# Performance work log

Hardware: AMD Instinct MI355X
Metric: run time of the kernel (lower is better)

Reference implementation:

```python
import math
import jax, jax.numpy as jnp
import numpy as np

NUM_HEADS = 32
NUM_KV_HEADS = 8
HEAD_SIZE = 128
FEATURE_DIM = 64
SEQ_LEN = 2048
WINDOW_SIZE = 64
EPS = 1e-12
MASK_VALUE = -100000000.0


def _make_masks(n: int, w: int):
    # block-diagonal ones(w,w) tiles, plus the rolled (sub-diagonal) tiles
    m = math.ceil(n / w)
    mask = np.kron(np.eye(m), np.ones((w, w)))
    mask = mask + np.roll(mask, -w, axis=-1)
    mask = mask[:n, :n]
    mask_window = np.tril(mask).astype(bool)[None, None]          # [1,1,n,n]
    mask_linear = np.tril(1.0 - mask).astype(bool)[None, None]    # [1,1,n,n]
    return jnp.asarray(mask_window), jnp.asarray(mask_linear)


def _feature_map(w, x):
    # f(x) = clamp(cat(softmax(xW), softmax(-xW)), min=eps)
    z = jnp.einsum('hdf,bhld->bhlf', w, x)
    return jnp.clip(
        jnp.concatenate([jax.nn.softmax(z, axis=-1), jax.nn.softmax(-z, axis=-1)], axis=-1),
        EPS, None)


def setup_inputs() -> dict:
    key = jax.random.key(0)
    ks = jax.random.split(key, 6)
    return {
        'query': jax.random.normal(ks[0], (SEQ_LEN, NUM_HEADS * HEAD_SIZE), dtype=jnp.float32),
        'key': jax.random.normal(ks[1], (SEQ_LEN, NUM_KV_HEADS * HEAD_SIZE), dtype=jnp.float32),
        'value': jax.random.normal(ks[2], (SEQ_LEN, NUM_KV_HEADS * HEAD_SIZE), dtype=jnp.float32),
        'fmap_q_w': 0.02 * jax.random.normal(ks[3], (NUM_HEADS, HEAD_SIZE, FEATURE_DIM), dtype=jnp.float32),
        'fmap_k_w': 0.02 * jax.random.normal(ks[4], (NUM_HEADS, HEAD_SIZE, FEATURE_DIM), dtype=jnp.float32),
        'window_factors': jax.random.normal(ks[5], (1, NUM_HEADS, 1, 1), dtype=jnp.float32),
    }


def reference(query, key, value, fmap_q_w, fmap_k_w, window_factors):
    T = query.shape[0]
    q = query.reshape(T, NUM_HEADS, HEAD_SIZE)
    k = key.reshape(T, NUM_KV_HEADS, HEAD_SIZE)
    v = value.reshape(T, NUM_KV_HEADS, HEAD_SIZE)
    rep = NUM_HEADS // NUM_KV_HEADS
    k = jnp.repeat(k, rep, axis=1)
    v = jnp.repeat(v, rep, axis=1)
    # [T,H,D] -> [1,H,T,D]
    q = jnp.moveaxis(q, 0, -2)[None]
    k = jnp.moveaxis(k, 0, -2)[None]
    v = jnp.moveaxis(v, 0, -2)[None]

    f_q = _feature_map(fmap_q_w, q)  # [1,H,T,2F]
    f_k = _feature_map(fmap_k_w, k)
    wf = jax.nn.sigmoid(window_factors)

    mask_window, mask_linear = _make_masks(SEQ_LEN, WINDOW_SIZE)
    mask_window = mask_window[:, :, :T, :T]
    mask_linear = mask_linear[:, :, :T, :T]

    # sliding-window softmax term
    a_sm = jnp.einsum('bhmd,bhnd->bhmn', q, k) * (HEAD_SIZE ** -0.5)
    a_sm = jnp.where(mask_window, a_sm, MASK_VALUE)
    a_sm_max = jnp.max(a_sm, axis=-1, keepdims=True)
    a_sm = wf * jnp.exp(a_sm - a_sm_max)
    sum_sm = jnp.sum(a_sm, axis=-1, keepdims=True)

    # linear feature-map term (linear_factor = 1)
    a_ln = jnp.einsum('bhmd,bhnd->bhmn', f_q, f_k)
    a_ln = jnp.where(mask_linear, a_ln, 0.0)
    sum_ln = jnp.sum(a_ln, axis=-1, keepdims=True)

    y = jnp.einsum('bhmn,bhnd->bhmd', a_sm + a_ln, v)
    return y / (sum_sm + sum_ln)
```

## Files before the change

### kernel.cpp

```cpp
#include <hip/hip_runtime.h>
#include <math.h>

#define T_SEQ 2048
#define NH    32
#define NKV   8
#define HS    128
#define FD    64
#define NBLK  32
#define SCAN_NB 30
#define EPSF  1e-12f
#define LDP   136
#define STP   129

typedef unsigned short u16;
typedef __bf16 bf16x8 __attribute__((ext_vector_type(8)));
typedef float  f32x4  __attribute__((ext_vector_type(4)));

__device__ __forceinline__ u16 f2b(float f) {
  unsigned u = __builtin_bit_cast(unsigned, f);
  return (u16)((u + 0x7fffu + ((u >> 16) & 1u)) >> 16);
}

#define FKT_OFF 0
#define ST_OFF  16777216
#define VT_OFF  54525952
#define WT_OFF  58720256
#define KB_OFF  59768832

__device__ __forceinline__ void stage_bf(u16* buf, const u16* __restrict__ src, int tid) {
#pragma unroll
  for (int i = 0; i < 4; ++i) {
    int idx = tid * 8 + i * 2048, rr = idx >> 7, c = idx & 127;
    *(uint4*)(buf + rr * LDP + c) = *(const uint4*)(src + idx);
  }
}
__device__ __forceinline__ void stage_vt(u16* buf, const u16* __restrict__ vts,
                                         int rofs, int kb0, int B, int tid) {
#pragma unroll
  for (int i = 0; i < 4; ++i) {
    int idx = tid * 8 + i * 2048, rr = idx >> 7, c = idx & 127;
    int key = (c < 64) ? (kb0 * 64 + c) : (B * 64 + (c - 64));
    *(uint4*)(buf + rr * LDP + c) = *(const uint4*)(vts + (size_t)(rr + rofs) * T_SEQ + key);
  }
}

__global__ __launch_bounds__(256) void k_prep(
    const float* __restrict__ wq, const float* __restrict__ wk,
    const float* __restrict__ vg, const float* __restrict__ kg,
    u16* __restrict__ WT, u16* __restrict__ VT,
    u16* __restrict__ FKT, u16* __restrict__ KBB)
{
  __shared__ __align__(16) u16 smem[2 * 64 * 136];
  const int bx = blockIdx.x, tid = threadIdx.x;
  const int lane = tid & 63, w = tid >> 6;
  const int quad = lane >> 4, txn = lane & 15;

  if (bx < 32) {
    float* sB = (float*)smem;
    const float* src = wq + (size_t)bx * HS * FD;
    for (int idx = tid * 4; idx < 8192; idx += 1024) {
      int r = idx >> 6, c = idx & 63;
      *(float4*)(sB + r * 68 + c) = *(const float4*)(src + idx);
    }
    __syncthreads();
    u16* dst = WT + (size_t)bx * 8192;
    for (int i = 0; i < 8; ++i) {
      int ch = tid + i * 256;
      int f = ch >> 5, d4 = (ch & 31) * 4;
      ushort4 u;
      u.x = f2b(sB[(d4 + 0) * 68 + f]);
      u.y = f2b(sB[(d4 + 1) * 68 + f]);
      u.z = f2b(sB[(d4 + 2) * 68 + f]);
      u.w = f2b(sB[(d4 + 3) * 68 + f]);
      *(ushort4*)(dst + f * 128 + d4) = u;
    }
    return;
  }

  if (bx < 288) {
    const int idx2 = bx - 32;
    const int b = idx2 & 31, kvh = idx2 >> 5;
    float* sV = (float*)smem;
    for (int idx = tid * 4; idx < 8192; idx += 1024) {
      int r = idx >> 7, c = idx & 127;
      *(float4*)(sV + r * 129 + c) = *(const float4*)(vg + (size_t)(b * 64 + r) * (NKV * HS) + kvh * HS + c);
    }
    __syncthreads();
#pragma unroll
    for (int i = 0; i < 32; ++i) {
      int d = w * 32 + i;
      VT[((size_t)(kvh * 128 + d)) * T_SEQ + b * 64 + lane] = f2b(sV[lane * 129 + d]);
    }
    return;
  }

  const int j2 = bx - 288;
  const int lt = j2 & 31, h = j2 >> 5;
  u16* sX = smem;
  u16* sW = smem + 64 * 136;

  const float* xbase = kg + (h >> 2) * HS;
  const int    xstr  = NKV * HS;
  for (int idx = tid * 4; idx < 8192; idx += 1024) {
    int r = idx >> 7, c = idx & 127;
    float4 v4 = *(const float4*)(xbase + (size_t)(lt * 64 + r) * xstr + c);
    ushort4 u; u.x = f2b(v4.x); u.y = f2b(v4.y); u.z = f2b(v4.z); u.w = f2b(v4.w);
    *(ushort4*)(sX + r * 136 + c) = u;
  }
  {
    const float* wsrc = wk + (size_t)h * (HS * FD);
    const int d = tid >> 1, f0 = (tid & 1) * 32;
#pragma unroll
    for (int i = 0; i < 8; ++i) {
      float4 v4 = *(const float4*)(wsrc + d * 64 + f0 + i * 4);
      sW[(f0 + i * 4 + 0) * 136 + d] = f2b(v4.x);
      sW[(f0 + i * 4 + 1) * 136 + d] = f2b(v4.y);
      sW[(f0 + i * 4 + 2) * 136 + d] = f2b(v4.z);
      sW[(f0 + i * 4 + 3) * 136 + d] = f2b(v4.w);
    }
  }
  __syncthreads();

  if ((h & 3) == 0) {
    u16* ob = KBB + ((size_t)((h >> 2) * NBLK + lt)) * 8192;
    for (int i = 0; i < 4; ++i) {
      int ch = tid + i * 256;
      int row = ch >> 4, d8 = (ch & 15) * 8;
      *(uint4*)(ob + row * 128 + d8) = *(const uint4*)(sX + row * 136 + d8);
    }
  }

  const int arow = w * 16 + txn;
  const f32x4 vzero = {0.f, 0.f, 0.f, 0.f};
  f32x4 zt[4] = {vzero, vzero, vzero, vzero};
#pragma unroll
  for (int ks = 0; ks < 4; ++ks) {
    bf16x8 a = *(const bf16x8*)(sX + arow * 136 + ks * 32 + quad * 8);
#pragma unroll
    for (int nt = 0; nt < 4; ++nt) {
      bf16x8 bb = *(const bf16x8*)(sW + (nt * 16 + txn) * 136 + ks * 32 + quad * 8);
      zt[nt] = __builtin_amdgcn_mfma_f32_16x16x32_bf16(a, bb, zt[nt], 0, 0, 0);
    }
  }

  float E1[4][4], E2[4][4];
#pragma unroll
  for (int r = 0; r < 4; ++r) {
    float zv[4];
    float mx = -1e30f, mn = 1e30f;
#pragma unroll
    for (int nt = 0; nt < 4; ++nt) {
      zv[nt] = zt[nt][r];
      mx = fmaxf(mx, zv[nt]); mn = fminf(mn, zv[nt]);
    }
#pragma unroll
    for (int o = 1; o < 16; o <<= 1) {
      mx = fmaxf(mx, __shfl_xor(mx, o));
      mn = fminf(mn, __shfl_xor(mn, o));
    }
    float e1[4], e2[4], s1 = 0.f, s2 = 0.f;
#pragma unroll
    for (int nt = 0; nt < 4; ++nt) {
      e1[nt] = __expf(zv[nt] - mx); s1 += e1[nt];
      e2[nt] = __expf(mn - zv[nt]); s2 += e2[nt];
    }
#pragma unroll
    for (int o = 1; o < 16; o <<= 1) { s1 += __shfl_xor(s1, o); s2 += __shfl_xor(s2, o); }
    float r1 = 1.f / s1, r2 = 1.f / s2;
#pragma unroll
    for (int nt = 0; nt < 4; ++nt) {
      E1[r][nt] = fmaxf(e1[nt] * r1, EPSF);
      E2[r][nt] = fmaxf(e2[nt] * r2, EPSF);
    }
  }

  __syncthreads();

#pragma unroll
  for (int r = 0; r < 4; ++r) {
    int j = w * 16 + quad * 4 + r;
#pragma unroll
    for (int nt = 0; nt < 4; ++nt) {
      sX[(nt * 16 + txn) * 68 + j]        = f2b(E1[r][nt]);
      sX[(nt * 16 + txn + 64) * 68 + j]   = f2b(E2[r][nt]);
    }
  }
  __syncthreads();
  u16* ob = FKT + ((size_t)(h * 32 + lt)) * 8192;
  for (int i = 0; i < 8; ++i) {
    int ch = tid + i * 256;
    int row = ch >> 4, j4 = (ch & 15) * 4;
    *(ushort4*)(ob + row * 64 + j4) = *(const ushort4*)(sX + row * 68 + j4);
  }
}

__global__ __launch_bounds__(256) void k_scan(
    const u16* __restrict__ FKT, const u16* __restrict__ VT, u16* __restrict__ ST)
{
  __shared__ __align__(16) u16 sVT[2][16 * 72];
  __shared__ __align__(16) u16 sFK[2][64 * 72];
  const int L = blockIdx.x + 8 * blockIdx.y + 16 * blockIdx.z;
  const int xcd = L & 7, j = L >> 3;
  const int hsub = j & 3, fh = (j >> 2) & 1, dc = j >> 3;
  const int h = xcd * 4 + hsub;
  const int tid = threadIdx.x, lane = tid & 63, w = tid >> 6;
  const int quad = lane >> 4, txn = lane & 15;
  const bool doz = (dc == 0);

  bf16x8 vone;
#pragma unroll
  for (int jj = 0; jj < 8; ++jj) vone[jj] = (__bf16)1.0f;

  const u16* vbase = VT + ((size_t)((h >> 2) * 128 + dc * 16)) * T_SEQ;
  const u16* fbase = FKT + (size_t)(h * 32) * 8192 + fh * 4096;

  const int srow = tid >> 4, sj4 = (tid & 15) * 4;
  ushort4 rv, rf[4];
  rv = *(const ushort4*)(vbase + (size_t)srow * T_SEQ + sj4);
#pragma unroll
  for (int i = 0; i < 4; ++i) {
    int ch = tid + i * 256;
    int fr = ch >> 4, fj4 = (ch & 15) * 4;
    rf[i] = *(const ushort4*)(fbase + fr * 64 + fj4);
  }

  const f32x4 vzero = {0.f, 0.f, 0.f, 0.f};
  f32x4 acc = vzero, zacc = vzero;
  int cur = 0;

  for (int b = 0; b < SCAN_NB; ++b) {
    u16* dV = sVT[cur];
    u16* dF = sFK[cur];
    *(ushort4*)(dV + srow * 72 + sj4) = rv;
#pragma unroll
    for (int i = 0; i < 4; ++i) {
      int ch = tid + i * 256;
      int fr = ch >> 4, fj4 = (ch & 15) * 4;
      *(ushort4*)(dF + fr * 72 + fj4) = rf[i];
    }
    __syncthreads();
    if (b + 1 < SCAN_NB) {
      rv = *(const ushort4*)(vbase + (size_t)srow * T_SEQ + (b + 1) * 64 + sj4);
#pragma unroll
      for (int i = 0; i < 4; ++i) {
        int ch = tid + i * 256;
        int fr = ch >> 4, fj4 = (ch & 15) * 4;
        rf[i] = *(const ushort4*)(fbase + (size_t)(b + 1) * 8192 + fr * 64 + fj4);
      }
    }
#pragma unroll
    for (int ks = 0; ks < 2; ++ks) {
      bf16x8 a  = *(const bf16x8*)(dV + txn * 72 + ks * 32 + quad * 8);
      bf16x8 bb = *(const bf16x8*)(dF + (w * 16 + txn) * 72 + ks * 32 + quad * 8);
      acc = __builtin_amdgcn_mfma_f32_16x16x32_bf16(a, bb, acc, 0, 0, 0);
      if (doz) zacc = __builtin_amdgcn_mfma_f32_16x16x32_bf16(vone, bb, zacc, 0, 0, 0);
    }
    u16* Sb = ST + (((size_t)(h * NBLK + b)) * STP + dc * 16) * 128 + fh * 64;
#pragma unroll
    for (int r = 0; r < 4; ++r)
      Sb[(quad * 4 + r) * 128 + w * 16 + txn] = f2b(acc[r]);
    if (doz && quad == 0)
      ST[(((size_t)(h * NBLK + b)) * STP + 128) * 128 + fh * 64 + w * 16 + txn] = f2b(zacc[0]);
    cur ^= 1;
  }
}

__global__ __launch_bounds__(256, 4) void k_main(
    const float* __restrict__ qg, const u16* __restrict__ KBB,
    const u16* __restrict__ WT, const u16* __restrict__ ST,
    const u16* __restrict__ VT, const float* __restrict__ wfac,
    float* __restrict__ out)
{
  __shared__ __align__(16) u16 RA[64 * LDP];
  __shared__ __align__(16) u16 RB[64 * LDP];
  __shared__ __align__(16) u16 sz[128];
  const int L = blockIdx.x + 32 * blockIdx.y;
  const int xcd = L & 7, jj = L >> 3;
  const int hsub = jj & 3, B = jj >> 2;
  const int h = xcd * 4 + hsub;
  const int tid = threadIdx.x;
  const int lane = tid & 63, w = tid >> 6;
  const int quad = lane >> 4, txn = lane & 15;
  const int arow = w * 16 + txn;
  const int koff = quad * 8;

  const f32x4 vzero = {0.f, 0.f, 0.f, 0.f};
  f32x4 y[8];
#pragma unroll
  for (int t = 0; t < 8; ++t) y[t] = vzero;
  float sln[4] = {0.f, 0.f, 0.f, 0.f};
  const bf16x8 bzero = {0, 0, 0, 0, 0, 0, 0, 0};

  const int kb0 = (B >= 1) ? B - 1 : 0;
  const u16* ktB = KBB + ((size_t)((h >> 2) * NBLK + B)) * 8192;
  const u16* ktP = KBB + ((size_t)((h >> 2) * NBLK + kb0)) * 8192;
  const u16* vts = VT  + (size_t)((h >> 2) * 128) * T_SEQ;
  const u16* wqt = WT  + (size_t)h * 8192;
  const u16* ssrc = ST + ((size_t)(h * NBLK + (B >= 2 ? B - 2 : 0))) * (STP * 128);

  {
    const float* qb = qg + (size_t)(B * 64 + w * 16) * (NH * HS) + h * HS;
#pragma unroll
    for (int i = 0; i < 8; ++i) {
      int idx = lane + i * 64;
      int r = idx >> 5, c4 = (idx & 31) * 4;
      float4 v4 = *(const float4*)(qb + (size_t)r * (NH * HS) + c4);
      ushort4 u; u.x = f2b(v4.x); u.y = f2b(v4.y); u.z = f2b(v4.z); u.w = f2b(v4.w);
      *(ushort4*)(RA + (w * 16 + r) * LDP + c4) = u;
    }
  }
  stage_bf(RB, ktB, tid);

  f32x4 zt[4] = {vzero, vzero, vzero, vzero};
  if (B >= 2) {
#pragma unroll
    for (int ks = 0; ks < 4; ++ks) {
      bf16x8 a = *(const bf16x8*)(RA + arow * LDP + ks * 32 + koff);
#pragma unroll
      for (int nt = 0; nt < 4; ++nt) {
        bf16x8 bb = *(const bf16x8*)(wqt + (nt * 16 + txn) * 128 + ks * 32 + koff);
        zt[nt] = __builtin_amdgcn_mfma_f32_16x16x32_bf16(a, bb, zt[nt], 0, 0, 0);
      }
    }
  }

  unsigned Epk[4][4];
  if (B >= 2) {
#pragma unroll
    for (int r = 0; r < 4; ++r) {
      float zv[4];
      float mx = -1e30f, mn = 1e30f;
#pragma unroll
      for (int nt = 0; nt < 4; ++nt) {
        zv[nt] = zt[nt][r];
        mx = fmaxf(mx, zv[nt]); mn = fminf(mn, zv[nt]);
      }
#pragma unroll
      for (int o = 1; o < 16; o <<= 1) {
        mx = fmaxf(mx, __shfl_xor(mx, o));
        mn = fminf(mn, __shfl_xor(mn, o));
      }
      float e1[4], e2[4], s1 = 0.f, s2 = 0.f;
#pragma unroll
      for (int nt = 0; nt < 4; ++nt) {
        e1[nt] = __expf(zv[nt] - mx); s1 += e1[nt];
        e2[nt] = __expf(mn - zv[nt]); s2 += e2[nt];
      }
#pragma unroll
      for (int o = 1; o < 16; o <<= 1) { s1 += __shfl_xor(s1, o); s2 += __shfl_xor(s2, o); }
      float r1 = 1.f / s1, r2 = 1.f / s2;
#pragma unroll
      for (int nt = 0; nt < 4; ++nt) {
        unsigned lo = f2b(fmaxf(e1[nt] * r1, EPSF));
        unsigned hi = f2b(fmaxf(e2[nt] * r2, EPSF));
        Epk[r][nt] = lo | (hi << 16);
      }
    }
  }
  __syncthreads();

  f32x4 s[8];
#pragma unroll
  for (int t = 0; t < 8; ++t) s[t] = vzero;
#pragma unroll
  for (int ks = 0; ks < 4; ++ks) {
    bf16x8 a = *(const bf16x8*)(RA + arow * LDP + ks * 32 + koff);
#pragma unroll
    for (int t = 0; t < 4; ++t) {
      bf16x8 bb = *(const bf16x8*)(RB + (t * 16 + txn) * LDP + ks * 32 + koff);
      s[4 + t] = __builtin_amdgcn_mfma_f32_16x16x32_bf16(a, bb, s[4 + t], 0, 0, 0);
    }
  }

  if (B >= 1) {
    __syncthreads();
    stage_bf(RB, ktP, tid);
    __syncthreads();
#pragma unroll
    for (int ks = 0; ks < 4; ++ks) {
      bf16x8 a = *(const bf16x8*)(RA + arow * LDP + ks * 32 + koff);
#pragma unroll
      for (int t = 0; t < 4; ++t) {
        bf16x8 bb = *(const bf16x8*)(RB + (t * 16 + txn) * LDP + ks * 32 + koff);
        s[t] = __builtin_amdgcn_mfma_f32_16x16x32_bf16(a, bb, s[t], 0, 0, 0);
      }
    }
  }

  float wf = wfac[h];
  wf = 1.f / (1.f + __expf(-wf));
  const float scale = 0.08838834764831845f;
  float ssum[4];
#pragma unroll
  for (int r = 0; r < 4; ++r) {
    const int irow = w * 16 + quad * 4 + r;
    float sv[8];
    float m = -1e30f;
#pragma unroll
    for (int t = 0; t < 8; ++t) {
      float x = s[t][r] * scale;
      bool msk = (t < 4) ? (B == 0) : ((t - 4) * 16 + txn > irow);
      x = msk ? -1e30f : x;
      sv[t] = x;
      m = fmaxf(m, x);
    }
#pragma unroll
    for (int o = 1; o < 16; o <<= 1) m = fmaxf(m, __shfl_xor(m, o));
    float ss = 0.f;
#pragma unroll
    for (int t = 0; t < 8; ++t) {
      float e = (sv[t] > -1e29f) ? wf * __expf(sv[t] - m) : 0.f;
      ss += e;
      RA[irow * LDP + t * 16 + txn] = f2b(e);
    }
#pragma unroll
    for (int o = 1; o < 16; o <<= 1) ss += __shfl_xor(ss, o);
    ssum[r] = ss;
  }
  __syncthreads();

  stage_vt(RB, vts, 0, kb0, B, tid);
  __syncthreads();
#pragma unroll
  for (int ks = 0; ks < 4; ++ks) {
    if (B == 0 && ks < 2) continue;
    bf16x8 a = *(const bf16x8*)(RA + arow * LDP + ks * 32 + koff);
#pragma unroll
    for (int t = 0; t < 4; ++t) {
      bf16x8 bb = *(const bf16x8*)(RB + (t * 16 + txn) * LDP + ks * 32 + koff);
      y[t] = __builtin_amdgcn_mfma_f32_16x16x32_bf16(a, bb, y[t], 0, 0, 0);
    }
  }
  __syncthreads();

  stage_vt(RB, vts, 64, kb0, B, tid);
  __syncthreads();
#pragma unroll
  for (int ks = 0; ks < 4; ++ks) {
    if (B == 0 && ks < 2) continue;
    bf16x8 a = *(const bf16x8*)(RA + arow * LDP + ks * 32 + koff);
#pragma unroll
    for (int t = 4; t < 8; ++t) {
      bf16x8 bb = *(const bf16x8*)(RB + (t * 16 + txn - 64) * LDP + ks * 32 + koff);
      y[t] = __builtin_amdgcn_mfma_f32_16x16x32_bf16(a, bb, y[t], 0, 0, 0);
    }
  }

  if (B >= 2) {
    __syncthreads();
#pragma unroll
    for (int r = 0; r < 4; ++r) {
      int row = w * 16 + quad * 4 + r;
#pragma unroll
      for (int nt = 0; nt < 4; ++nt) {
        RA[row * LDP + nt * 16 + txn]      = (u16)(Epk[r][nt] & 0xffffu);
        RA[row * LDP + 64 + nt * 16 + txn] = (u16)(Epk[r][nt] >> 16);
      }
    }
    stage_bf(RB, ssrc, tid);
    if (tid < 32) *(ushort4*)(sz + tid * 4) = *(const ushort4*)(ssrc + 16384 + tid * 4);
    __syncthreads();
    f32x4 yz = vzero;
#pragma unroll
    for (int ks = 0; ks < 4; ++ks) {
      bf16x8 a = *(const bf16x8*)(RA + arow * LDP + ks * 32 + koff);
#pragma unroll
      for (int t = 0; t < 4; ++t) {
        bf16x8 bb = *(const bf16x8*)(RB + (t * 16 + txn) * LDP + ks * 32 + koff);
        y[t] = __builtin_amdgcn_mfma_f32_16x16x32_bf16(a, bb, y[t], 0, 0, 0);
      }
      bf16x8 bz = (txn == 0) ? *(const bf16x8*)(sz + ks * 32 + koff) : bzero;
      yz = __builtin_amdgcn_mfma_f32_16x16x32_bf16(a, bz, yz, 0, 0, 0);
    }
    __syncthreads();
    stage_bf(RB, ssrc + 8192, tid);
    __syncthreads();
#pragma unroll
    for (int ks = 0; ks < 4; ++ks) {
      bf16x8 a = *(const bf16x8*)(RA + arow * LDP + ks * 32 + koff);
#pragma unroll
      for (int t = 4; t < 8; ++t) {
        bf16x8 bb = *(const bf16x8*)(RB + (t * 16 + txn - 64) * LDP + ks * 32 + koff);
        y[t] = __builtin_amdgcn_mfma_f32_16x16x32_bf16(a, bb, y[t], 0, 0, 0);
      }
    }
#pragma unroll
    for (int r = 0; r < 4; ++r) sln[r] = __shfl(yz[r], lane & 48);
  }

  const size_t obase = ((size_t)h * T_SEQ + B * 64) * HS;
#pragma unroll
  for (int r = 0; r < 4; ++r) {
    float inv = 1.f / (ssum[r] + sln[r]);
    int irow = w * 16 + quad * 4 + r;
#pragma unroll
    for (int t = 0; t < 8; ++t)
      out[obase + (size_t)irow * HS + t * 16 + txn] = y[t][r] * inv;
  }
}

extern "C" void kernel_launch(void* const* d_in, const int* in_sizes, int n_in,
                              void* d_out, int out_size, void* d_ws, size_t ws_size,
                              hipStream_t stream) {
  const float* q    = (const float*)d_in[0];
  const float* k    = (const float*)d_in[1];
  const float* v    = (const float*)d_in[2];
  const float* wq   = (const float*)d_in[3];
  const float* wk   = (const float*)d_in[4];
  const float* wfac = (const float*)d_in[5];
  float* out = (float*)d_out;
  char* wsb = (char*)d_ws;

  u16* FKT = (u16*)(wsb + FKT_OFF);
  u16* ST  = (u16*)(wsb + ST_OFF);
  u16* VT  = (u16*)(wsb + VT_OFF);
  u16* WT  = (u16*)(wsb + WT_OFF);
  u16* KBB = (u16*)(wsb + KB_OFF);

  k_prep <<<dim3(1312),     256, 0, stream>>>(wq, wk, v, k, WT, VT, FKT, KBB);
  k_scan <<<dim3(8, 2, NH), 256, 0, stream>>>(FKT, VT, ST);
  k_main <<<dim3(NBLK, NH), 256, 0, stream>>>(q, KBB, WT, ST, VT, wfac, out);
}
```

Measured before the change: 160.3 us.

## Enlarge k_main shared staging buffer to load full 128-row tiles at once

Replaces the 64-row RB staging buffer with a 128-row BB buffer so that both key blocks, both halves of V^T, and both halves of the state matrix are each staged in a single pass. This removes several __syncthreads barriers and load/compute serialisation points, and the V^T staging is issued before the softmax computation so it overlaps with it. In exchange, LDS per block roughly doubles and launch bounds drop from 4 to 3 blocks per CU, which may lower occupancy.

```diff
diff --git a/kernel.cpp b/kernel.cpp
--- a/kernel.cpp
+++ b/kernel.cpp
@@ -26,23 +26,6 @@
 #define VT_OFF  54525952
 #define WT_OFF  58720256
 #define KB_OFF  59768832
-
-__device__ __forceinline__ void stage_bf(u16* buf, const u16* __restrict__ src, int tid) {
-#pragma unroll
-  for (int i = 0; i < 4; ++i) {
-    int idx = tid * 8 + i * 2048, rr = idx >> 7, c = idx & 127;
-    *(uint4*)(buf + rr * LDP + c) = *(const uint4*)(src + idx);
-  }
-}
-__device__ __forceinline__ void stage_vt(u16* buf, const u16* __restrict__ vts,
-                                         int rofs, int kb0, int B, int tid) {
-#pragma unroll
-  for (int i = 0; i < 4; ++i) {
-    int idx = tid * 8 + i * 2048, rr = idx >> 7, c = idx & 127;
-    int key = (c < 64) ? (kb0 * 64 + c) : (B * 64 + (c - 64));
-    *(uint4*)(buf + rr * LDP + c) = *(const uint4*)(vts + (size_t)(rr + rofs) * T_SEQ + key);
-  }
-}
 
 __global__ __launch_bounds__(256) void k_prep(
     const float* __restrict__ wq, const float* __restrict__ wk,
@@ -265,14 +248,14 @@
   }
 }
 
-__global__ __launch_bounds__(256, 4) void k_main(
+__global__ __launch_bounds__(256, 3) void k_main(
     const float* __restrict__ qg, const u16* __restrict__ KBB,
     const u16* __restrict__ WT, const u16* __restrict__ ST,
     const u16* __restrict__ VT, const float* __restrict__ wfac,
     float* __restrict__ out)
 {
   __shared__ __align__(16) u16 RA[64 * LDP];
-  __shared__ __align__(16) u16 RB[64 * LDP];
+  __shared__ __align__(16) u16 BB[128 * LDP];
   __shared__ __align__(16) u16 sz[128];
   const int L = blockIdx.x + 32 * blockIdx.y;
   const int xcd = L & 7, jj = L >> 3;
@@ -285,10 +268,6 @@
   const int koff = quad * 8;
 
   const f32x4 vzero = {0.f, 0.f, 0.f, 0.f};
-  f32x4 y[8];
-#pragma unroll
-  for (int t = 0; t < 8; ++t) y[t] = vzero;
-  float sln[4] = {0.f, 0.f, 0.f, 0.f};
   const bf16x8 bzero = {0, 0, 0, 0, 0, 0, 0, 0};
 
   const int kb0 = (B >= 1) ? B - 1 : 0;
@@ -309,7 +288,12 @@
       *(ushort4*)(RA + (w * 16 + r) * LDP + c4) = u;
     }
   }
-  stage_bf(RB, ktB, tid);
+#pragma unroll
+  for (int i = 0; i < 8; ++i) {
+    int idx = tid * 8 + i * 2048, rr = idx >> 7, c = idx & 127;
+    const u16* src = (rr < 64) ? (ktB + rr * 128 + c) : (ktP + (rr - 64) * 128 + c);
+    *(uint4*)(BB + rr * LDP + c) = *(const uint4*)(src);
+  }
 
   f32x4 zt[4] = {vzero, vzero, vzero, vzero};
   if (B >= 2) {
@@ -323,7 +307,6 @@
       }
     }
   }
-
   unsigned Epk[4][4];
   if (B >= 2) {
 #pragma unroll
@@ -367,26 +350,25 @@
     bf16x8 a = *(const bf16x8*)(RA + arow * LDP + ks * 32 + koff);
 #pragma unroll
     for (int t = 0; t < 4; ++t) {
-      bf16x8 bb = *(const bf16x8*)(RB + (t * 16 + txn) * LDP + ks * 32 + koff);
+      bf16x8 bb = *(const bf16x8*)(BB + (t * 16 + txn) * LDP + ks * 32 + koff);
       s[4 + t] = __builtin_amdgcn_mfma_f32_16x16x32_bf16(a, bb, s[4 + t], 0, 0, 0);
     }
-  }
-
-  if (B >= 1) {
-    __syncthreads();
-    stage_bf(RB, ktP, tid);
-    __syncthreads();
-#pragma unroll
-    for (int ks = 0; ks < 4; ++ks) {
-      bf16x8 a = *(const bf16x8*)(RA + arow * LDP + ks * 32 + koff);
+    if (B >= 1) {
 #pragma unroll
       for (int t = 0; t < 4; ++t) {
-        bf16x8 bb = *(const bf16x8*)(RB + (t * 16 + txn) * LDP + ks * 32 + koff);
+        bf16x8 bb = *(const bf16x8*)(BB + (64 + t * 16 + txn) * LDP + ks * 32 + koff);
         s[t] = __builtin_amdgcn_mfma_f32_16x16x32_bf16(a, bb, s[t], 0, 0, 0);
       }
     }
   }
-
+  __syncthreads();
+
+#pragma unroll
+  for (int i = 0; i < 8; ++i) {
+    int idx = tid * 8 + i * 2048, rr = idx >> 7, c = idx & 127;
+    int key = (c < 64) ? (kb0 * 64 + c) : (B * 64 + (c - 64));
+    *(uint4*)(BB + rr * LDP + c) = *(const uint4*)(vts + (size_t)rr * T_SEQ + key);
+  }
   float wf = wfac[h];
   wf = 1.f / (1.f + __expf(-wf));
   const float scale = 0.08838834764831845f;
@@ -419,35 +401,29 @@
   }
   __syncthreads();
 
-  stage_vt(RB, vts, 0, kb0, B, tid);
-  __syncthreads();
+  f32x4 y[8];
+#pragma unroll
+  for (int t = 0; t < 8; ++t) y[t] = vzero;
 #pragma unroll
   for (int ks = 0; ks < 4; ++ks) {
     if (B == 0 && ks < 2) continue;
     bf16x8 a = *(const bf16x8*)(RA + arow * LDP + ks * 32 + koff);
 #pragma unroll
-    for (int t = 0; t < 4; ++t) {
-      bf16x8 bb = *(const bf16x8*)(RB + (t * 16 + txn) * LDP + ks * 32 + koff);
+    for (int t = 0; t < 8; ++t) {
+      bf16x8 bb = *(const bf16x8*)(BB + (t * 16 + txn) * LDP + ks * 32 + koff);
       y[t] = __builtin_amdgcn_mfma_f32_16x16x32_bf16(a, bb, y[t], 0, 0, 0);
     }
   }
   __syncthreads();
 
-  stage_vt(RB, vts, 64, kb0, B, tid);
-  __syncthreads();
-#pragma unroll
-  for (int ks = 0; ks < 4; ++ks) {
-    if (B == 0 && ks < 2) continue;
-    bf16x8 a = *(const bf16x8*)(RA + arow * LDP + ks * 32 + koff);
-#pragma unroll
-    for (int t = 4; t < 8; ++t) {
-      bf16x8 bb = *(const bf16x8*)(RB + (t * 16 + txn - 64) * LDP + ks * 32 + koff);
-      y[t] = __builtin_amdgcn_mfma_f32_16x16x32_bf16(a, bb, y[t], 0, 0, 0);
-    }
-  }
-
+  float sln[4] = {0.f, 0.f, 0.f, 0.f};
   if (B >= 2) {
-    __syncthreads();
+#pragma unroll
+    for (int i = 0; i < 8; ++i) {
+      int idx = tid * 8 + i * 2048, rr = idx >> 7, c = idx & 127;
+      *(uint4*)(BB + rr * LDP + c) = *(const uint4*)(ssrc + rr * 128 + c);
+    }
+    if (tid < 32) *(ushort4*)(sz + tid * 4) = *(const ushort4*)(ssrc + 16384 + tid * 4);
 #pragma unroll
     for (int r = 0; r < 4; ++r) {
       int row = w * 16 + quad * 4 + r;
@@ -457,32 +433,18 @@
         RA[row * LDP + 64 + nt * 16 + txn] = (u16)(Epk[r][nt] >> 16);
       }
     }
-    stage_bf(RB, ssrc, tid);
-    if (tid < 32) *(ushort4*)(sz + tid * 4) = *(const ushort4*)(ssrc + 16384 + tid * 4);
     __syncthreads();
     f32x4 yz = vzero;
 #pragma unroll
     for (int ks = 0; ks < 4; ++ks) {
       bf16x8 a = *(const bf16x8*)(RA + arow * LDP + ks * 32 + koff);
 #pragma unroll
-      for (int t = 0; t < 4; ++t) {
-        bf16x8 bb = *(const bf16x8*)(RB + (t * 16 + txn) * LDP + ks * 32 + koff);
+      for (int t = 0; t < 8; ++t) {
+        bf16x8 bb = *(const bf16x8*)(BB + (t * 16 + txn) * LDP + ks * 32 + koff);
         y[t] = __builtin_amdgcn_mfma_f32_16x16x32_bf16(a, bb, y[t], 0, 0, 0);
       }
       bf16x8 bz = (txn == 0) ? *(const bf16x8*)(sz + ks * 32 + koff) : bzero;
       yz = __builtin_amdgcn_mfma_f32_16x16x32_bf16(a, bz, yz, 0, 0, 0);
-    }
-    __syncthreads();
-    stage_bf(RB, ssrc + 8192, tid);
-    __syncthreads();
-#pragma unroll
-    for (int ks = 0; ks < 4; ++ks) {
-      bf16x8 a = *(const bf16x8*)(RA + arow * LDP + ks * 32 + koff);
-#pragma unroll
-      for (int t = 4; t < 8; ++t) {
-        bf16x8 bb = *(const bf16x8*)(RB + (t * 16 + txn - 64) * LDP + ks * 32 + koff);
-        y[t] = __builtin_amdgcn_mfma_f32_16x16x32_bf16(a, bb, y[t], 0, 0, 0);
-      }
     }
 #pragma unroll
     for (int r = 0; r < 4; ++r) sln[r] = __shfl(yz[r], lane & 48);
```

Result: no change. 160.7 us (+0.3%).
